# Performance work log

Hardware: AMD Instinct MI355X
Metric: run time of the kernel (lower is better)

Reference implementation:

```python
import jax, jax.numpy as jnp
import numpy as np


def setup_inputs() -> dict:
    key = jax.random.key(0)
    k1, k2 = jax.random.split(key)
    B, HW, C, M, P = 8, 4096, 1024, 32, 512
    feature_map = jax.random.normal(k1, (B, HW, C), dtype=jnp.float32)
    # normalized (y, x) coords in [0,1], as produced by mask.nonzero()/[H,W]
    point_coords = jax.random.uniform(k2, (B, M, P, 2), dtype=jnp.float32)
    return {"feature_map": feature_map, "point_coords": point_coords}


def reference(feature_map, point_coords):
    # feature_map: [B, H*W, C]; point_coords: [B, M, P, 2] as (y_norm, x_norm).
    B, HW, C = feature_map.shape
    h = w = int(np.sqrt(HW))
    # torch flips coords to (x, y); grid_sample(align_corners=True) maps
    # grid g = 2*coord-1 to pixel coord*(size-1).
    y = point_coords[..., 0] * (h - 1)  # [B, M, P]
    x = point_coords[..., 1] * (w - 1)
    x0f = jnp.floor(x)
    y0f = jnp.floor(y)
    wx = (x - x0f)[..., None]  # [B, M, P, 1]
    wy = (y - y0f)[..., None]
    ix0 = jnp.clip(x0f.astype(jnp.int32), 0, w - 1)
    ix1 = jnp.clip(ix0 + 1, 0, w - 1)
    iy0 = jnp.clip(y0f.astype(jnp.int32), 0, h - 1)
    iy1 = jnp.clip(iy0 + 1, 0, h - 1)

    def gather(iy, ix):
        idx = (iy * w + ix).reshape(B, -1)  # [B, M*P]
        g = jnp.take_along_axis(feature_map, idx[:, :, None], axis=1)  # [B, M*P, C]
        return g.reshape(B, iy.shape[1], iy.shape[2], C)

    f00 = gather(iy0, ix0)
    f01 = gather(iy0, ix1)
    f10 = gather(iy1, ix0)
    f11 = gather(iy1, ix1)
    # bilinear interpolation -> [B, M, P, C]
    sampled = (f00 * (1 - wx) * (1 - wy) + f01 * wx * (1 - wy)
               + f10 * (1 - wx) * wy + f11 * wx * wy)
    # AdaptiveAvgPool1d(1) over points, then transpose -> [B, M, 1, C]
    region_feat = jnp.mean(sampled, axis=2, keepdims=True)
    return region_feat
```

## Files before the change

### kernel.cpp

```cpp
#include <hip/hip_runtime.h>


#define NB 8
#define NM 32
#define NP 512
#define NC 1024
#define NH 64
#define NHW 4096

#define KC    128
#define NKC   (NHW / KC)
#define MT    8
#define CTILE 256
#define NCT   (NC / CTILE)
#define SEG   16
#define NSEG  (KC / SEG)
#define FS4   (NC / 4)

__global__ __launch_bounds__(256) void scatter_w(
    const float* __restrict__ pc, float* __restrict__ W)
{
    int idx = blockIdx.x * 256 + threadIdx.x;
    int bm  = idx >> 9;
    int m   = bm & (NM - 1);
    int b   = bm >> 5;

    float2 c = ((const float2*)pc)[idx];
    float y = c.x * 63.0f;
    float x = c.y * 63.0f;
    float x0f = floorf(x), y0f = floorf(y);
    float wx = x - x0f, wy = y - y0f;
    int ix0 = min(max((int)x0f, 0), 63);
    int ix1 = min(ix0 + 1, 63);
    int iy0 = min(max((int)y0f, 0), 63);
    int iy1 = min(iy0 + 1, 63);
    float wx1 = 1.0f - wx, wy1 = 1.0f - wy;
    const float s = 1.0f / (float)NP;

    float* Wb = W + (size_t)b * (NHW * NM) + m;
    atomicAdd(Wb + ((iy0 * NH + ix0) * NM), wx1 * wy1 * s);
    atomicAdd(Wb + ((iy0 * NH + ix1) * NM), wx  * wy1 * s);
    atomicAdd(Wb + ((iy1 * NH + ix0) * NM), wx1 * wy  * s);
    atomicAdd(Wb + ((iy1 * NH + ix1) * NM), wx  * wy  * s);
}

__global__ __launch_bounds__(256, 2) void wgemm(
    const float* __restrict__ W, const float* __restrict__ F,
    float* __restrict__ P)
{
    __shared__ float sW[KC * NM];

    const int kc   = blockIdx.x;
    const int ct   = blockIdx.y;
    const int b    = blockIdx.z;
    const int tid  = threadIdx.x;
    const int mq   = tid >> 6;
    const int lane = tid & 63;
    const int hw0  = kc * KC;

    {
        const float4* Wg = (const float4*)(W + ((size_t)b * NHW + hw0) * NM);
        float4* sW4 = (float4*)sW;
#pragma unroll
        for (int j = 0; j < 4; ++j)
            sW4[tid + 256 * j] = Wg[tid + 256 * j];
    }
    __syncthreads();

    const float4* __restrict__ Fb =
        (const float4*)(F + ((size_t)b * NHW + hw0) * NC + ct * CTILE) + lane;

    float4 acc[MT];
#pragma unroll
    for (int m = 0; m < MT; ++m) acc[m] = make_float4(0.f, 0.f, 0.f, 0.f);

    const float* sWq = sW + mq * MT;

#define STEP(r, fv)                                                        \
    do {                                                                   \
        const float* wr_ = sWq + (r) * NM;                                 \
        float4 w0_ = *(const float4*)(wr_);                                \
        float4 w1_ = *(const float4*)(wr_ + 4);                            \
        const float wm_[MT] = { w0_.x, w0_.y, w0_.z, w0_.w,                \
                                w1_.x, w1_.y, w1_.z, w1_.w };              \
        _Pragma("unroll")                                                  \
        for (int m_ = 0; m_ < MT; ++m_) {                                  \
            float w_ = wm_[m_];                                            \
            acc[m_].x = fmaf(w_, (fv).x, acc[m_].x);                       \
            acc[m_].y = fmaf(w_, (fv).y, acc[m_].y);                       \
            acc[m_].z = fmaf(w_, (fv).z, acc[m_].z);                       \
            acc[m_].w = fmaf(w_, (fv).w, acc[m_].w);                       \
        }                                                                  \
    } while (0)

    float4 bufA[SEG], bufB[SEG];

#pragma unroll
    for (int j = 0; j < SEG; ++j) bufA[j] = Fb[j * FS4];

#pragma unroll
    for (int s = 0; s < NSEG; s += 2) {
        if (s + 1 < NSEG) {
#pragma unroll
            for (int j = 0; j < SEG; ++j)
                bufB[j] = Fb[((s + 1) * SEG + j) * FS4];
        }
#pragma unroll
        for (int j = 0; j < SEG; ++j) STEP(s * SEG + j, bufA[j]);

        if (s + 2 < NSEG) {
#pragma unroll
            for (int j = 0; j < SEG; ++j)
                bufA[j] = Fb[((s + 2) * SEG + j) * FS4];
        }
        if (s + 1 < NSEG) {
#pragma unroll
            for (int j = 0; j < SEG; ++j) STEP((s + 1) * SEG + j, bufB[j]);
        }
    }
#undef STEP

    float* pb = P + (((size_t)kc * NB + b) * NM + mq * MT) * NC
              + ct * CTILE + 4 * lane;
#pragma unroll
    for (int mm = 0; mm < MT; ++mm)
        *(float4*)(pb + (size_t)mm * NC) = acc[mm];
}

__global__ __launch_bounds__(256) void reduce_p(
    const float* __restrict__ P, float* __restrict__ out)
{
    const int idx = blockIdx.x * 256 + threadIdx.x;
    const float4* p4 = (const float4*)P;
    const int stride = NB * NM * NC / 4;
    float4 s = make_float4(0.f, 0.f, 0.f, 0.f);
#pragma unroll
    for (int kc = 0; kc < NKC; ++kc) {
        float4 v = p4[(size_t)kc * stride + idx];
        s.x += v.x; s.y += v.y; s.z += v.z; s.w += v.w;
    }
    ((float4*)out)[idx] = s;
}

__global__ __launch_bounds__(256) void region_pool_direct(
    const float* __restrict__ fm, const float* __restrict__ pc,
    float* __restrict__ out)
{
    __shared__ int4   sIdx[NP];
    __shared__ float4 sWt[NP];
    const int bid = blockIdx.x;
    const int b   = bid >> 5;
    const int tid = threadIdx.x;
    const float2* pc2 = (const float2*)(pc + (size_t)bid * NP * 2);
    for (int p = tid; p < NP; p += 256) {
        float2 c = pc2[p];
        float y = c.x * 63.0f, x = c.y * 63.0f;
        float x0f = floorf(x), y0f = floorf(y);
        float wx = x - x0f, wy = y - y0f;
        int ix0 = min(max((int)x0f, 0), 63);
        int ix1 = min(ix0 + 1, 63);
        int iy0 = min(max((int)y0f, 0), 63);
        int iy1 = min(iy0 + 1, 63);
        sIdx[p] = make_int4((iy0 * NH + ix0) << 10, (iy0 * NH + ix1) << 10,
                            (iy1 * NH + ix0) << 10, (iy1 * NH + ix1) << 10);
        float wx1 = 1.0f - wx, wy1 = 1.0f - wy;
        sWt[p] = make_float4(wx1 * wy1, wx * wy1, wx1 * wy, wx * wy);
    }
    __syncthreads();
    const float* Fb = fm + (size_t)b * (NHW * NC) + tid * 4;
    float4 acc = make_float4(0.f, 0.f, 0.f, 0.f);
#pragma unroll 4
    for (int p = 0; p < NP; ++p) {
        int4 off = sIdx[p]; float4 w = sWt[p];
        float4 f00 = *(const float4*)(Fb + off.x);
        float4 f01 = *(const float4*)(Fb + off.y);
        float4 f10 = *(const float4*)(Fb + off.z);
        float4 f11 = *(const float4*)(Fb + off.w);
        acc.x = fmaf(w.x, f00.x, fmaf(w.y, f01.x, fmaf(w.z, f10.x, fmaf(w.w, f11.x, acc.x))));
        acc.y = fmaf(w.x, f00.y, fmaf(w.y, f01.y, fmaf(w.z, f10.y, fmaf(w.w, f11.y, acc.y))));
        acc.z = fmaf(w.x, f00.z, fmaf(w.y, f01.z, fmaf(w.z, f10.z, fmaf(w.w, f11.z, acc.z))));
        acc.w = fmaf(w.x, f00.w, fmaf(w.y, f01.w, fmaf(w.z, f10.w, fmaf(w.w, f11.w, acc.w))));
    }
    const float inv = 1.0f / (float)NP;
    ((float4*)(out + (size_t)bid * NC))[tid] =
        make_float4(acc.x * inv, acc.y * inv, acc.z * inv, acc.w * inv);
}

extern "C" void kernel_launch(void* const* d_in, const int* in_sizes, int n_in,
                              void* d_out, int out_size, void* d_ws, size_t ws_size,
                              hipStream_t stream) {
    const float* fm = (const float*)d_in[0];
    const float* pc = (const float*)d_in[1];
    float* out = (float*)d_out;

    const size_t wbytes = (size_t)NB * NHW * NM * sizeof(float);
    const size_t pbytes = (size_t)NKC * NB * NM * NC * sizeof(float);
    if (ws_size >= wbytes + pbytes) {
        float* W = (float*)d_ws;
        float* P = (float*)((char*)d_ws + wbytes);
        hipMemsetAsync(W, 0, wbytes, stream);
        scatter_w<<<(NB * NM * NP) / 256, 256, 0, stream>>>(pc, W);
        dim3 grid(NKC, NCT, NB);
        wgemm<<<grid, 256, 0, stream>>>(W, fm, P);
        reduce_p<<<(NB * NM * NC / 4) / 256, 256, 0, stream>>>(P, out);
    } else {
        region_pool_direct<<<NB * NM, 256, 0, stream>>>(fm, pc, out);
    }
}
```

Baseline: 234.0 us.

## Use packed FP32 FMA in wgemm and widen blocks to 512 threads

```diff
diff --git a/kernel.cpp b/kernel.cpp
--- a/kernel.cpp
+++ b/kernel.cpp
@@ -11,7 +11,7 @@
 #define KC    128
 #define NKC   (NHW / KC)
 #define MT    8
-#define CTILE 256
+#define CTILE 512
 #define NCT   (NC / CTILE)
 #define SEG   16
 #define NSEG  (KC / SEG)
@@ -44,52 +44,60 @@
     atomicAdd(Wb + ((iy1 * NH + ix1) * NM), wx  * wy  * s);
 }
 
-__global__ __launch_bounds__(256, 2) void wgemm(
+__global__ __launch_bounds__(512) void wgemm(
     const float* __restrict__ W, const float* __restrict__ F,
     float* __restrict__ P)
 {
-    __shared__ float sW[KC * NM];
+    __shared__ float sW2[KC * NM * 2];
 
     const int kc   = blockIdx.x;
     const int ct   = blockIdx.y;
     const int b    = blockIdx.z;
     const int tid  = threadIdx.x;
-    const int mq   = tid >> 6;
+    const int wid  = tid >> 6;
+    const int mq   = wid & 3;
+    const int ch   = wid >> 2;
     const int lane = tid & 63;
     const int hw0  = kc * KC;
 
     {
         const float4* Wg = (const float4*)(W + ((size_t)b * NHW + hw0) * NM);
-        float4* sW4 = (float4*)sW;
-#pragma unroll
-        for (int j = 0; j < 4; ++j)
-            sW4[tid + 256 * j] = Wg[tid + 256 * j];
+        float4* d = (float4*)sW2;
+#pragma unroll
+        for (int j = 0; j < 2; ++j) {
+            int i = tid + 512 * j;
+            float4 w = Wg[i];
+            d[2 * i]     = make_float4(w.x, w.x, w.y, w.y);
+            d[2 * i + 1] = make_float4(w.z, w.z, w.w, w.w);
+        }
     }
     __syncthreads();
 
     const float4* __restrict__ Fb =
-        (const float4*)(F + ((size_t)b * NHW + hw0) * NC + ct * CTILE) + lane;
-
-    float4 acc[MT];
-#pragma unroll
-    for (int m = 0; m < MT; ++m) acc[m] = make_float4(0.f, 0.f, 0.f, 0.f);
-
-    const float* sWq = sW + mq * MT;
-
-#define STEP(r, fv)                                                        \
+        (const float4*)(F + ((size_t)b * NHW + hw0) * NC
+                        + ct * CTILE + ch * 256) + lane;
+
+    float2 acc[MT][2];
+#pragma unroll
+    for (int m = 0; m < MT; ++m) {
+        acc[m][0] = make_float2(0.f, 0.f);
+        acc[m][1] = make_float2(0.f, 0.f);
+    }
+
+    const float* sWq = sW2 + mq * 16;
+
+#define STEP(r, f4v)                                                       \
     do {                                                                   \
-        const float* wr_ = sWq + (r) * NM;                                 \
-        float4 w0_ = *(const float4*)(wr_);                                \
-        float4 w1_ = *(const float4*)(wr_ + 4);                            \
-        const float wm_[MT] = { w0_.x, w0_.y, w0_.z, w0_.w,                \
-                                w1_.x, w1_.y, w1_.z, w1_.w };              \
+        const float* wr_ = sWq + (r) * 64;                                 \
+        float2 f01_ = make_float2((f4v).x, (f4v).y);                       \
+        float2 f23_ = make_float2((f4v).z, (f4v).w);                       \
         _Pragma("unroll")                                                  \
         for (int m_ = 0; m_ < MT; ++m_) {                                  \
-            float w_ = wm_[m_];                                            \
-            acc[m_].x = fmaf(w_, (fv).x, acc[m_].x);                       \
-            acc[m_].y = fmaf(w_, (fv).y, acc[m_].y);                       \
-            acc[m_].z = fmaf(w_, (fv).z, acc[m_].z);                       \
-            acc[m_].w = fmaf(w_, (fv).w, acc[m_].w);                       \
+            float2 wd_ = *(const float2*)(wr_ + 2 * m_);        \
+            asm("v_pk_fma_f32 %0, %1, %2, %0"                              \
+                : "+v"(acc[m_][0]) : "v"(wd_), "v"(f01_));                 \
+            asm("v_pk_fma_f32 %0, %1, %2, %0"                              \
+                : "+v"(acc[m_][1]) : "v"(wd_), "v"(f23_));                 \
         }                                                                  \
     } while (0)
 
@@ -121,10 +129,12 @@
 #undef STEP
 
     float* pb = P + (((size_t)kc * NB + b) * NM + mq * MT) * NC
-              + ct * CTILE + 4 * lane;
+              + ct * CTILE + ch * 256 + 4 * lane;
 #pragma unroll
     for (int mm = 0; mm < MT; ++mm)
-        *(float4*)(pb + (size_t)mm * NC) = acc[mm];
+        *(float4*)(pb + (size_t)mm * NC) =
+            make_float4(acc[mm][0].x, acc[mm][0].y,
+                        acc[mm][1].x, acc[mm][1].y);
 }
 
 __global__ __launch_bounds__(256) void reduce_p(
@@ -201,7 +211,7 @@
         hipMemsetAsync(W, 0, wbytes, stream);
         scatter_w<<<(NB * NM * NP) / 256, 256, 0, stream>>>(pc, W);
         dim3 grid(NKC, NCT, NB);
-        wgemm<<<grid, 256, 0, stream>>>(W, fm, P);
+        wgemm<<<grid, 512, 0, stream>>>(W, fm, P);
         reduce_p<<<(NB * NM * NC / 4) / 256, 256, 0, stream>>>(P, out);
     } else {
         region_pool_direct<<<NB * NM, 256, 0, stream>>>(fm, pc, out);
```

Result: slower. 245.2 us (+4.8%).
